# Kernel tuning notes

Measured on AMD Instinct MI355X. Metric: run time of the kernel, lower is better.

Reference implementation:

```python
import math
import jax, jax.numpy as jnp
import numpy as np

B, T, I, H = 32, 64, 256, 512
TAU = 20.0                      # tau_trace and membrane tau
DECAY = math.exp(-1.0 / TAU)    # exp trace decay (exp_convolve)
ALPHA = math.exp(-1.0 / TAU)    # leaky-integrator membrane decay
ETA = 0.1                       # Hebbian plasticity learning rate


def setup_inputs() -> dict:
    key = jax.random.key(0)
    kx, kw = jax.random.split(key)
    x = jax.random.normal(kx, (B, T, I), dtype=jnp.float32)
    # xavier_uniform with gain sqrt(2) ~ normal with matched std
    std = math.sqrt(2.0) * math.sqrt(2.0 / (2 * H + I))
    W = (jax.random.normal(kw, (2 * H, I), dtype=jnp.float32) * std)
    return {"x": x, "W": W}


def reference(x, W):
    """Write-mode (recall=False) forward of MemoryLayer.
    Returns (mem [B,H,H], keys [B,T,H], vals [B,T,H])."""
    h = W.shape[0] // 2
    b = x.shape[0]
    # i = linear(x, W): [B,T,2H], split into key/value drives
    i = jnp.einsum('bti,hi->bth', x, W)
    ik, iv = i[..., :h], i[..., h:]

    mem0 = jnp.zeros((b, h, h), x.dtype)
    z = jnp.zeros((b, h), x.dtype)

    def step(carry, inp):
        kv, vv, kt, vt, mem = carry
        ik_t, iv_t = inp
        # key neuron dynamics: leaky integration + tanh
        kv = ALPHA * kv + ik_t
        k = jnp.tanh(kv)
        # associative read: (key.unsqueeze(1) * mem).sum(2) == mem @ key
        ikv = 0.2 * jnp.einsum('bij,bj->bi', mem, k)
        # value neuron dynamics
        vv = ALPHA * vv + iv_t + ikv
        v = jnp.tanh(vv)
        # exp_convolve traces
        kt = DECAY * kt + (1.0 - DECAY) * k
        vt = DECAY * vt + (1.0 - DECAY) * v
        # Hebbian outer-product plasticity: delta_mem = eta * vt (x) kt
        mem = mem + ETA * jnp.einsum('bi,bj->bij', vt, kt)
        return (kv, vv, kt, vt, mem), (k, v)

    # scan over time (sequential recurrence), batch fully vectorized
    (kv, vv, kt, vt, mem), (ks, vs) = jax.lax.scan(
        step, (z, z, z, z, mem0),
        (jnp.swapaxes(ik, 0, 1), jnp.swapaxes(iv, 0, 1)))
    keys = jnp.swapaxes(ks, 0, 1)  # [B,T,H]
    vals = jnp.swapaxes(vs, 0, 1)  # [B,T,H]
    return mem, keys, vals
```

## Files before the change

### kernel.cpp

```cpp
#include <hip/hip_runtime.h>

#define B_ 32
#define T_ 64
#define I_ 256
#define H_ 512

static constexpr float ALPHA_F = 0.951229424500714f;
static constexpr float OMD_F   = 0.048770575499286f;
static constexpr float ETA_F   = 0.1f;
static constexpr float CSCALE  = 0.02f;

__device__ __forceinline__ float tanh_fast(float x) {
  float xc = fminf(fmaxf(x, -15.f), 15.f);
  float e = __expf(2.f * xc);
  return (e - 1.f) * __builtin_amdgcn_rcpf(e + 1.f);
}

template <int CTRL>
__device__ __forceinline__ float dpp_add(float x) {
  int mv = __builtin_amdgcn_update_dpp(0, __float_as_int(x), CTRL, 0xF, 0xF, true);
  return x + __int_as_float(mv);
}
__device__ __forceinline__ float wave_sum_dpp(float x) {
  x = dpp_add<0x111>(x);
  x = dpp_add<0x112>(x);
  x = dpp_add<0x114>(x);
  x = dpp_add<0x118>(x);
  x = dpp_add<0x142>(x);
  x = dpp_add<0x143>(x);
  return x;
}

__global__ __launch_bounds__(256) void proj_kscan(const float* __restrict__ x,
                                                  const float* __restrict__ W,
                                                  float* __restrict__ keys,
                                                  float* __restrict__ ktg,
                                                  float* __restrict__ ivbuf) {
  __shared__ float Ak[64][68];
  __shared__ float Bk[64][68];
  const int b  = blockIdx.x;
  const int n0 = blockIdx.y * 64;
  const int m0 = b * 64;
  const int tid = threadIdx.x;
  const int ty = tid >> 4, tx = tid & 15;
  const int sr = tid >> 2;
  const int sc = tid & 3;
  float acc[4][4] = {};

  for (int k0 = 0; k0 < I_; k0 += 64) {
#pragma unroll
    for (int e = 0; e < 4; ++e) {
      const int cq = sc + 4 * e;
      float4 xv = *reinterpret_cast<const float4*>(&x[(size_t)(m0 + sr) * I_ + k0 + cq * 4]);
      Ak[cq * 4 + 0][sr] = xv.x;
      Ak[cq * 4 + 1][sr] = xv.y;
      Ak[cq * 4 + 2][sr] = xv.z;
      Ak[cq * 4 + 3][sr] = xv.w;
      float4 wv = *reinterpret_cast<const float4*>(&W[(size_t)(n0 + sr) * I_ + k0 + cq * 4]);
      Bk[cq * 4 + 0][sr] = wv.x;
      Bk[cq * 4 + 1][sr] = wv.y;
      Bk[cq * 4 + 2][sr] = wv.z;
      Bk[cq * 4 + 3][sr] = wv.w;
    }
    __syncthreads();
#pragma unroll 8
    for (int kk = 0; kk < 64; ++kk) {
      float4 a4 = *reinterpret_cast<const float4*>(&Ak[kk][ty * 4]);
      float4 b4 = *reinterpret_cast<const float4*>(&Bk[kk][tx * 4]);
      float av[4] = {a4.x, a4.y, a4.z, a4.w};
      float bv[4] = {b4.x, b4.y, b4.z, b4.w};
#pragma unroll
      for (int i = 0; i < 4; ++i)
#pragma unroll
        for (int j = 0; j < 4; ++j) acc[i][j] += av[i] * bv[j];
    }
    __syncthreads();
  }

  if (n0 < 512) {
    float* scr = &Ak[0][0];
#pragma unroll
    for (int i = 0; i < 4; ++i)
#pragma unroll
      for (int j = 0; j < 4; ++j) scr[(ty * 4 + i) * 68 + tx * 4 + j] = acc[i][j];
    __syncthreads();
    if (tid < 64) {
      float kv = 0.f, kt = 0.f;
      float* ko  = keys + (size_t)b * T_ * H_ + n0 + tid;
      float* kto = ktg  + (size_t)b * T_ * H_ + n0 + tid;
#pragma unroll 8
      for (int t = 0; t < T_; ++t) {
        kv = ALPHA_F * kv + scr[t * 68 + tid];
        float k = tanh_fast(kv);
        kt = ALPHA_F * kt + OMD_F * k;
        ko[(size_t)t * H_]  = k;
        kto[(size_t)t * H_] = kt;
      }
    }
  } else {
    const int hv0 = n0 - 512;
#pragma unroll
    for (int i = 0; i < 4; ++i)
      *reinterpret_cast<float4*>(&ivbuf[((size_t)b * T_ + ty * 4 + i) * H_ + hv0 + tx * 4]) =
          make_float4(acc[i][0], acc[i][1], acc[i][2], acc[i][3]);
  }
}

__global__ __launch_bounds__(512) void dots_kernel(const float* __restrict__ keys,
                                                   const float* __restrict__ ktg,
                                                   float* __restrict__ C) {
  const int b = blockIdx.y;
  const int t = blockIdx.x * 8 + (threadIdx.x >> 6);
  const int lane = threadIdx.x & 63;
  const float* krow = keys + ((size_t)b * T_ + t) * H_ + 4 * lane;
  float4 k0 = *reinterpret_cast<const float4*>(krow);
  float4 k1 = *reinterpret_cast<const float4*>(krow + 256);
  const float* tb = ktg + (size_t)b * T_ * H_ + 4 * lane;
  float* Cb = C + ((size_t)b * T_ + t) * T_;
#pragma unroll 8
  for (int s = 0; s < T_; ++s) {
    const float* ar = tb + (size_t)s * H_;
    float4 a0 = *reinterpret_cast<const float4*>(ar);
    float4 a1 = *reinterpret_cast<const float4*>(ar + 256);
    float p = a0.x * k0.x + a0.y * k0.y + a0.z * k0.z + a0.w * k0.w
            + a1.x * k1.x + a1.y * k1.y + a1.z * k1.z + a1.w * k1.w;
    p = wave_sum_dpp(p);
    if (lane == 63) Cb[s] = CSCALE * p;
  }
}

#define IVG(T) (((T) & 3) == 0 ? ivq[(T) >> 2].x : ((T) & 3) == 1 ? ivq[(T) >> 2].y \
              : ((T) & 3) == 2 ? ivq[(T) >> 2].z : ivq[(T) >> 2].w)
#define VQSET(T, val) do { \
    if (((T) & 3) == 0)      vqv[(T) >> 2].x = (val); \
    else if (((T) & 3) == 1) vqv[(T) >> 2].y = (val); \
    else if (((T) & 3) == 2) vqv[(T) >> 2].z = (val); \
    else                     vqv[(T) >> 2].w = (val); } while (0)

#define VSTEP(TT, CUR, NXT)                                                   \
  {                                                                           \
    if ((TT) + 1 < T_) {                                                      \
      _Pragma("unroll")                                                       \
      for (int q = 0; q < 16; ++q)                                            \
        NXT[q] = *reinterpret_cast<const float4*>(&Cs[(TT) + 1][4 * q]);      \
    }                                                                         \
    float p0 = 0.f, p1 = 0.f, p2 = 0.f, p3 = 0.f;                             \
    _Pragma("unroll")                                                         \
    for (int q = 0; q < 16; ++q) {                                            \
      p0 += CUR[q].x * vqv[q].x;                                              \
      p1 += CUR[q].y * vqv[q].y;                                              \
      p2 += CUR[q].z * vqv[q].z;                                              \
      p3 += CUR[q].w * vqv[q].w;                                              \
    }                                                                         \
    float ikv = (p0 + p1) + (p2 + p3);                                        \
    vv = ALPHA_F * vv + IVG(TT) + ikv;                                        \
    float v = tanh_fast(vv);                                                  \
    vt = ALPHA_F * vt + OMD_F * v;                                            \
    VQSET(TT, vt);                                                            \
    vo[(size_t)(TT) * H_]  = v;                                               \
    vto[(size_t)(TT) * H_] = vt;                                              \
  }

#define VP2(T2) VSTEP(T2, ca, cbuf) VSTEP((T2) + 1, cbuf, ca)
#define VP8(T8) VP2(T8) VP2((T8) + 2) VP2((T8) + 4) VP2((T8) + 6)
#define IVLD(Q) { ivq[Q].x = pv[(size_t)(4 * (Q) + 0) * H_]; \
                  ivq[Q].y = pv[(size_t)(4 * (Q) + 1) * H_]; \
                  ivq[Q].z = pv[(size_t)(4 * (Q) + 2) * H_]; \
                  ivq[Q].w = pv[(size_t)(4 * (Q) + 3) * H_]; }

__global__ __launch_bounds__(64, 1) void vscan_kernel(const float* __restrict__ ivbuf,
                                                      const float* __restrict__ C,
                                                      float* __restrict__ vals,
                                                      float* __restrict__ vtg) {
  __shared__ float Cs[T_][T_];
  const int b    = blockIdx.x >> 3;
  const int lane = threadIdx.x;
  const int h    = ((blockIdx.x & 7) << 6) + lane;

  const float* Cb = C + (size_t)b * T_ * T_;
#pragma unroll
  for (int e = 0; e < 16; ++e)
    reinterpret_cast<float4*>(&Cs[0][0])[lane + (e << 6)] =
        reinterpret_cast<const float4*>(Cb)[lane + (e << 6)];

  const float* pv = ivbuf + (size_t)b * T_ * H_ + h;
  float* vo  = vals + ((size_t)b * T_) * H_ + h;
  float* vto = vtg  + ((size_t)b * T_) * H_ + h;

  float4 ivq[16];
  IVLD(0)  IVLD(1)  IVLD(2)  IVLD(3)  IVLD(4)  IVLD(5)  IVLD(6)  IVLD(7)
  IVLD(8)  IVLD(9)  IVLD(10) IVLD(11) IVLD(12) IVLD(13) IVLD(14) IVLD(15)

  float vv = 0.f, vt = 0.f;
  float4 vqv[16];
#pragma unroll
  for (int q = 0; q < 16; ++q) vqv[q] = make_float4(0.f, 0.f, 0.f, 0.f);

  __syncthreads();

  float4 ca[16], cbuf[16];
#pragma unroll
  for (int q = 0; q < 16; ++q)
    ca[q] = *reinterpret_cast<const float4*>(&Cs[0][4 * q]);

  VP8(0) VP8(8) VP8(16) VP8(24) VP8(32) VP8(40) VP8(48) VP8(56)
}

__global__ __launch_bounds__(256) void mem_gemm(const float* __restrict__ vtg,
                                                const float* __restrict__ ktg,
                                                float* __restrict__ mem) {
  const int b = blockIdx.z;
  const int i0 = blockIdx.y * 64;
  const int j0 = blockIdx.x * 64;
  __shared__ float Vs[64][68];
  __shared__ float Ks[64][68];
  const int tid = threadIdx.x;
  const int ty = tid >> 4, tx = tid & 15;
  const float* vb = vtg + (size_t)b * T_ * H_;
  const float* kb = ktg + (size_t)b * T_ * H_;
#pragma unroll
  for (int e = 0; e < 16; ++e) {
    int idx = tid + e * 256;
    int t = idx >> 6, c = idx & 63;
    Vs[t][c] = vb[(size_t)t * H_ + i0 + c];
    Ks[t][c] = kb[(size_t)t * H_ + j0 + c];
  }
  __syncthreads();
  float acc[4][4] = {};
#pragma unroll 8
  for (int t = 0; t < 64; ++t) {
    float4 a4 = *reinterpret_cast<const float4*>(&Vs[t][ty * 4]);
    float4 b4 = *reinterpret_cast<const float4*>(&Ks[t][tx * 4]);
    float av[4] = {a4.x, a4.y, a4.z, a4.w};
    float bv[4] = {b4.x, b4.y, b4.z, b4.w};
#pragma unroll
    for (int i = 0; i < 4; ++i)
#pragma unroll
      for (int j = 0; j < 4; ++j) acc[i][j] += av[i] * bv[j];
  }
  float* mb = mem + (size_t)b * H_ * H_;
#pragma unroll
  for (int i = 0; i < 4; ++i) {
    float4 o = make_float4(ETA_F * acc[i][0], ETA_F * acc[i][1],
                           ETA_F * acc[i][2], ETA_F * acc[i][3]);
    *reinterpret_cast<float4*>(&mb[(size_t)(i0 + ty * 4 + i) * H_ + j0 + tx * 4]) = o;
  }
}

extern "C" void kernel_launch(void* const* d_in, const int* in_sizes, int n_in,
                              void* d_out, int out_size, void* d_ws, size_t ws_size,
                              hipStream_t stream) {
  const float* x = (const float*)d_in[0];
  const float* W = (const float*)d_in[1];
  float* out = (float*)d_out;
  float* mem  = out;
  float* keys = out + (size_t)B_ * H_ * H_;
  float* vals = keys + (size_t)B_ * T_ * H_;

  float* ktg   = (float*)d_ws;
  float* ivbuf = ktg + (size_t)B_ * T_ * H_;
  float* vtg   = ivbuf + (size_t)B_ * T_ * H_;
  float* Cbuf  = vtg + (size_t)B_ * T_ * H_;

  proj_kscan<<<dim3(B_, 16), 256, 0, stream>>>(x, W, keys, ktg, ivbuf);
  dots_kernel<<<dim3(8, B_), 512, 0, stream>>>(keys, ktg, Cbuf);
  vscan_kernel<<<dim3(8 * B_), 64, 0, stream>>>(ivbuf, Cbuf, vals, vtg);
  mem_gemm<<<dim3(8, 8, B_), 256, 0, stream>>>(vtg, ktg, mem);
}
```

Before: 86.38 us.

## Compute memory outer-product sum with bf16 MFMA from transposed bf16 traces

The scan kernels now also write the key and value traces as bf16 in a transposed [B,H,T] layout, packed along time, and the vscan kernel no longer stores the fp32 value trace. The final mem GEMM is replaced by a kernel that uses the 16x16x32 bf16 MFMA instruction and reads operands straight from global memory, with no LDS staging. This targets the FP32 FMA cost and the trace traffic of the mem computation. In exchange, the mem output loses precision, which may matter for tolerance, and the output stores are scattered scalar writes.

```diff
diff --git a/kernel.cpp b/kernel.cpp
--- a/kernel.cpp
+++ b/kernel.cpp
@@ -10,10 +10,18 @@
 static constexpr float ETA_F   = 0.1f;
 static constexpr float CSCALE  = 0.02f;
 
+typedef __bf16 bf16x8 __attribute__((ext_vector_type(8)));
+typedef float  f32x4  __attribute__((ext_vector_type(4)));
+
 __device__ __forceinline__ float tanh_fast(float x) {
   float xc = fminf(fmaxf(x, -15.f), 15.f);
   float e = __expf(2.f * xc);
   return (e - 1.f) * __builtin_amdgcn_rcpf(e + 1.f);
+}
+__device__ __forceinline__ unsigned int f2bf(float f) {
+  unsigned int u = __float_as_uint(f);
+  u += 0x7fffu + ((u >> 16) & 1u);
+  return u >> 16;
 }
 
 template <int CTRL>
@@ -35,6 +43,7 @@
                                                   const float* __restrict__ W,
                                                   float* __restrict__ keys,
                                                   float* __restrict__ ktg,
+                                                  ushort* __restrict__ ktb16T,
                                                   float* __restrict__ ivbuf) {
   __shared__ float Ak[64][68];
   __shared__ float Bk[64][68];
@@ -86,16 +95,25 @@
     __syncthreads();
     if (tid < 64) {
       float kv = 0.f, kt = 0.f;
+      unsigned int kpk[32];
       float* ko  = keys + (size_t)b * T_ * H_ + n0 + tid;
       float* kto = ktg  + (size_t)b * T_ * H_ + n0 + tid;
-#pragma unroll 8
+#pragma unroll
       for (int t = 0; t < T_; ++t) {
         kv = ALPHA_F * kv + scr[t * 68 + tid];
         float k = tanh_fast(kv);
         kt = ALPHA_F * kt + OMD_F * k;
         ko[(size_t)t * H_]  = k;
         kto[(size_t)t * H_] = kt;
+        unsigned int us = f2bf(kt);
+        if ((t & 1) == 0) kpk[t >> 1] = us;
+        else              kpk[t >> 1] |= us << 16;
       }
+      ushort* kb = ktb16T + ((size_t)b * H_ + n0 + tid) * T_;
+#pragma unroll
+      for (int e = 0; e < 8; ++e)
+        reinterpret_cast<uint4*>(kb)[e] =
+            make_uint4(kpk[4 * e], kpk[4 * e + 1], kpk[4 * e + 2], kpk[4 * e + 3]);
     }
   } else {
     const int hv0 = n0 - 512;
@@ -157,8 +175,7 @@
     float v = tanh_fast(vv);                                                  \
     vt = ALPHA_F * vt + OMD_F * v;                                            \
     VQSET(TT, vt);                                                            \
-    vo[(size_t)(TT) * H_]  = v;                                               \
-    vto[(size_t)(TT) * H_] = vt;                                              \
+    vo[(size_t)(TT) * H_] = v;                                                \
   }
 
 #define VP2(T2) VSTEP(T2, ca, cbuf) VSTEP((T2) + 1, cbuf, ca)
@@ -171,7 +188,7 @@
 __global__ __launch_bounds__(64, 1) void vscan_kernel(const float* __restrict__ ivbuf,
                                                       const float* __restrict__ C,
                                                       float* __restrict__ vals,
-                                                      float* __restrict__ vtg) {
+                                                      ushort* __restrict__ vtb16T) {
   __shared__ float Cs[T_][T_];
   const int b    = blockIdx.x >> 3;
   const int lane = threadIdx.x;
@@ -184,8 +201,7 @@
         reinterpret_cast<const float4*>(Cb)[lane + (e << 6)];
 
   const float* pv = ivbuf + (size_t)b * T_ * H_ + h;
-  float* vo  = vals + ((size_t)b * T_) * H_ + h;
-  float* vto = vtg  + ((size_t)b * T_) * H_ + h;
+  float* vo = vals + ((size_t)b * T_) * H_ + h;
 
   float4 ivq[16];
   IVLD(0)  IVLD(1)  IVLD(2)  IVLD(3)  IVLD(4)  IVLD(5)  IVLD(6)  IVLD(7)
@@ -204,47 +220,45 @@
     ca[q] = *reinterpret_cast<const float4*>(&Cs[0][4 * q]);
 
   VP8(0) VP8(8) VP8(16) VP8(24) VP8(32) VP8(40) VP8(48) VP8(56)
-}
-
-__global__ __launch_bounds__(256) void mem_gemm(const float* __restrict__ vtg,
-                                                const float* __restrict__ ktg,
+
+  ushort* vb16 = vtb16T + ((size_t)b * H_ + h) * T_;
+#pragma unroll
+  for (int q = 0; q < 16; ++q) {
+    unsigned int u0 = f2bf(vqv[q].x) | (f2bf(vqv[q].y) << 16);
+    unsigned int u1 = f2bf(vqv[q].z) | (f2bf(vqv[q].w) << 16);
+    reinterpret_cast<uint2*>(vb16)[q] = make_uint2(u0, u1);
+  }
+}
+
+__global__ __launch_bounds__(256) void mem_mfma(const ushort* __restrict__ vtb16T,
+                                                const ushort* __restrict__ ktb16T,
                                                 float* __restrict__ mem) {
-  const int b = blockIdx.z;
+  const int b  = blockIdx.z;
   const int i0 = blockIdx.y * 64;
   const int j0 = blockIdx.x * 64;
-  __shared__ float Vs[64][68];
-  __shared__ float Ks[64][68];
   const int tid = threadIdx.x;
-  const int ty = tid >> 4, tx = tid & 15;
-  const float* vb = vtg + (size_t)b * T_ * H_;
-  const float* kb = ktg + (size_t)b * T_ * H_;
-#pragma unroll
-  for (int e = 0; e < 16; ++e) {
-    int idx = tid + e * 256;
-    int t = idx >> 6, c = idx & 63;
-    Vs[t][c] = vb[(size_t)t * H_ + i0 + c];
-    Ks[t][c] = kb[(size_t)t * H_ + j0 + c];
-  }
-  __syncthreads();
-  float acc[4][4] = {};
-#pragma unroll 8
-  for (int t = 0; t < 64; ++t) {
-    float4 a4 = *reinterpret_cast<const float4*>(&Vs[t][ty * 4]);
-    float4 b4 = *reinterpret_cast<const float4*>(&Ks[t][tx * 4]);
-    float av[4] = {a4.x, a4.y, a4.z, a4.w};
-    float bv[4] = {b4.x, b4.y, b4.z, b4.w};
-#pragma unroll
-    for (int i = 0; i < 4; ++i)
-#pragma unroll
-      for (int j = 0; j < 4; ++j) acc[i][j] += av[i] * bv[j];
-  }
+  const int w = tid >> 6, l = tid & 63;
+  const int lrow = l & 15, lk8 = (l >> 4) * 8;
+
+  const ushort* ar = vtb16T + ((size_t)b * H_ + i0 + w * 16 + lrow) * T_ + lk8;
+  const ushort* br = ktb16T + ((size_t)b * H_ + j0 + lrow) * T_ + lk8;
+  f32x4 acc[4] = {};
+#pragma unroll
+  for (int ks = 0; ks < 2; ++ks) {
+    bf16x8 a = *reinterpret_cast<const bf16x8*>(ar + ks * 32);
+#pragma unroll
+    for (int jt = 0; jt < 4; ++jt) {
+      bf16x8 bv = *reinterpret_cast<const bf16x8*>(br + (size_t)jt * 16 * T_ + ks * 32);
+      acc[jt] = __builtin_amdgcn_mfma_f32_16x16x32_bf16(a, bv, acc[jt], 0, 0, 0);
+    }
+  }
+  const int tr0 = (l >> 4) * 4, tc = lrow;
   float* mb = mem + (size_t)b * H_ * H_;
 #pragma unroll
-  for (int i = 0; i < 4; ++i) {
-    float4 o = make_float4(ETA_F * acc[i][0], ETA_F * acc[i][1],
-                           ETA_F * acc[i][2], ETA_F * acc[i][3]);
-    *reinterpret_cast<float4*>(&mb[(size_t)(i0 + ty * 4 + i) * H_ + j0 + tx * 4]) = o;
-  }
+  for (int jt = 0; jt < 4; ++jt)
+#pragma unroll
+    for (int r = 0; r < 4; ++r)
+      mb[((size_t)i0 + w * 16 + tr0 + r) * H_ + j0 + jt * 16 + tc] = ETA_F * acc[jt][r];
 }
 
 extern "C" void kernel_launch(void* const* d_in, const int* in_sizes, int n_in,
@@ -257,13 +271,14 @@
   float* keys = out + (size_t)B_ * H_ * H_;
   float* vals = keys + (size_t)B_ * T_ * H_;
 
-  float* ktg   = (float*)d_ws;
-  float* ivbuf = ktg + (size_t)B_ * T_ * H_;
-  float* vtg   = ivbuf + (size_t)B_ * T_ * H_;
-  float* Cbuf  = vtg + (size_t)B_ * T_ * H_;
-
-  proj_kscan<<<dim3(B_, 16), 256, 0, stream>>>(x, W, keys, ktg, ivbuf);
+  float*  ktg    = (float*)d_ws;
+  float*  ivbuf  = ktg + (size_t)B_ * T_ * H_;
+  ushort* ktb16T = (ushort*)(ivbuf + (size_t)B_ * T_ * H_);
+  ushort* vtb16T = ktb16T + (size_t)B_ * H_ * T_;
+  float*  Cbuf   = (float*)(vtb16T + (size_t)B_ * H_ * T_);
+
+  proj_kscan<<<dim3(B_, 16), 256, 0, stream>>>(x, W, keys, ktg, ktb16T, ivbuf);
   dots_kernel<<<dim3(8, B_), 512, 0, stream>>>(keys, ktg, Cbuf);
-  vscan_kernel<<<dim3(8 * B_), 64, 0, stream>>>(ivbuf, Cbuf, vals, vtg);
-  mem_gemm<<<dim3(8, 8, B_), 256, 0, stream>>>(vtg, ktg, mem);
-}
+  vscan_kernel<<<dim3(8 * B_), 64, 0, stream>>>(ivbuf, Cbuf, vals, vtb16T);
+  mem_mfma<<<dim3(8, 8, B_), 256, 0, stream>>>(vtb16T, ktb16T, mem);
+}
```

Result: slower. 90.36 us (+4.6%).
